# Performance work log

Measured on AMD Instinct MI355X. Metric: run time of the kernel, lower is better.

## Reference

```python
import jax, jax.numpy as jnp
import numpy as np

N_NODES = 200000
N_EDGES = 6400000
IN_DIM = 15      # pfc_input_dim
POS_DIM = 4      # positional_dim
OUT_DIM = 2      # vtx_classes + 1


def setup_inputs() -> dict:
    key = jax.random.key(0)
    k1, k2, k3, k4, k5, k6, k7 = jax.random.split(key, 7)
    x_pfc = jax.random.normal(k1, (N_NODES, IN_DIM), dtype=jnp.float32)
    edge_index = jax.random.randint(k2, (2, N_EDGES), 0, N_NODES, dtype=jnp.int64)
    s_in = 1.0 / np.sqrt(IN_DIM)
    s_pos = 1.0 / np.sqrt(POS_DIM)
    # PointTransformerConv params: lin, lin_src, lin_dst (no bias), pos_nn = Linear(4, 2)
    W_lin = jax.random.uniform(k3, (OUT_DIM, IN_DIM), jnp.float32, -s_in, s_in)
    W_src = jax.random.uniform(k4, (OUT_DIM, IN_DIM), jnp.float32, -s_in, s_in)
    W_dst = jax.random.uniform(k5, (OUT_DIM, IN_DIM), jnp.float32, -s_in, s_in)
    W_pos = jax.random.uniform(k6, (OUT_DIM, POS_DIM), jnp.float32, -s_pos, s_pos)
    b_pos = jax.random.uniform(k7, (OUT_DIM,), jnp.float32, -s_pos, s_pos)
    return {"x_pfc": x_pfc, "edge_index": edge_index, "W_lin": W_lin,
            "W_src": W_src, "W_dst": W_dst, "W_pos": W_pos, "b_pos": b_pos}


def reference(x_pfc, edge_index, W_lin, W_src, W_dst, W_pos, b_pos):
    n = x_pfc.shape[0]
    pos = x_pfc[:, :POS_DIM]
    # original forward calls ptc_only(x, pos, edge_index.flip(0)):
    # source j = edge_index[1], target i = edge_index[0]
    j = edge_index[1]
    i = edge_index[0]
    # node-level linear maps (N x OUT_DIM)
    v = x_pfc @ W_lin.T
    a_src = x_pfc @ W_src.T
    a_dst = x_pfc @ W_dst.T
    # positional MLP on relative positions (E x OUT_DIM)
    delta = (pos[i] - pos[j]) @ W_pos.T + b_pos
    alpha = a_dst[i] - a_src[j] + delta
    # segment softmax over incoming edges of each target node i
    m = jax.ops.segment_max(alpha, i, num_segments=n)  # -inf for empty segments (never indexed)
    e = jnp.exp(alpha - m[i])
    denom = jax.ops.segment_sum(e, i, num_segments=n)
    attn = e / (denom[i] + 1e-16)
    msg = attn * (v[j] + delta)
    return jax.ops.segment_sum(msg, i, num_segments=n)
```

## Files before the change

kernel.cpp:

```cpp
#include <hip/hip_runtime.h>

#define N_NODES 200000
#define N_EDGES 6400000
#define IN_DIM 15
#define POS_DIM 4

#define CSHIFT 9
#define CMASK 511
#define NCOARSE ((N_NODES + 511) >> 9)
#define CHUNK 16384
#define NBLK ((N_EDGES + CHUNK - 1) / CHUNK)
#define CAP 17408

typedef unsigned uv4 __attribute__((ext_vector_type(4)));
typedef int      iv4 __attribute__((ext_vector_type(4)));


__global__ void node_prep(const float* __restrict__ x,
                          const float* __restrict__ Wlin,
                          const float* __restrict__ Wsrc,
                          const float* __restrict__ Wpos,
                          float4* __restrict__ tabJ,
                          unsigned* __restrict__ gcnt)
{
    int n = blockIdx.x * blockDim.x + threadIdx.x;
    if (n < NCOARSE) gcnt[n] = 0u;
    if (n >= N_NODES) return;
    const float* xp = x + (long)n * IN_DIM;
    float xv[IN_DIM];
#pragma unroll
    for (int k = 0; k < IN_DIM; ++k) xv[k] = xp[k];

    float p0 = 0.f, p1 = 0.f;
#pragma unroll
    for (int k = 0; k < POS_DIM; ++k) {
        p0 += Wpos[k] * xv[k];
        p1 += Wpos[POS_DIM + k] * xv[k];
    }
    float v0 = 0.f, v1 = 0.f, as0 = 0.f, as1 = 0.f;
#pragma unroll
    for (int k = 0; k < IN_DIM; ++k) {
        float xk = xv[k];
        v0  += Wlin[k] * xk;  v1  += Wlin[IN_DIM + k] * xk;
        as0 += Wsrc[k] * xk;  as1 += Wsrc[IN_DIM + k] * xk;
    }
    tabJ[n] = make_float4(as0 + p0, as1 + p1, v0 - p0, v1 - p1);
}

__global__ __launch_bounds__(512) void
scatter_kernel(const int* __restrict__ idx,
               unsigned* __restrict__ gcnt,
               unsigned* __restrict__ packed)
{
    __shared__ unsigned stage[CHUNK];
    __shared__ unsigned cnt[512];
    __shared__ unsigned lloc[512];
    __shared__ unsigned gdst[NCOARSE];
    __shared__ unsigned wsum[8];
    int b = blockIdx.x;
    int t = threadIdx.x;
    int lane = t & 63, wid = t >> 6;
    long s0 = (long)b * CHUNK;
    int end = (int)min((long)CHUNK, (long)N_EDGES - s0);
    cnt[t] = 0u;
    __syncthreads();
    iv4 myi[8];
    {
        int rr = 0;
        for (int e = t * 4; e < end; e += 2048, ++rr) {
            iv4 iv = __builtin_nontemporal_load((const iv4*)(idx + s0 + e));
            myi[rr] = iv;
            atomicAdd(&cnt[iv.x >> CSHIFT], 1u);
            atomicAdd(&cnt[iv.y >> CSHIFT], 1u);
            atomicAdd(&cnt[iv.z >> CSHIFT], 1u);
            atomicAdd(&cnt[iv.w >> CSHIFT], 1u);
        }
    }
    __syncthreads();
    unsigned v = cnt[t];
    unsigned s = v;
#pragma unroll
    for (int off = 1; off < 64; off <<= 1) {
        unsigned u = __shfl_up(s, off, 64);
        if (lane >= off) s += u;
    }
    if (lane == 63) wsum[wid] = s;
    __syncthreads();
    unsigned woff = 0;
#pragma unroll
    for (int w = 0; w < 8; ++w) woff += (w < wid) ? wsum[w] : 0u;
    {
        unsigned ex = woff + s - v;
        lloc[t] = ex;
        cnt[t] = ex;
        if (t < NCOARSE) gdst[t] = atomicAdd(&gcnt[t], v);
    }
    __syncthreads();
    {
        int rr = 0;
        for (int e = t * 4; e < end; e += 2048, ++rr) {
            iv4 iv = myi[rr];
            iv4 jv = __builtin_nontemporal_load((const iv4*)(idx + N_EDGES + s0 + e));
            unsigned r0 = atomicAdd(&cnt[iv.x >> CSHIFT], 1u);
            unsigned r1 = atomicAdd(&cnt[iv.y >> CSHIFT], 1u);
            unsigned r2 = atomicAdd(&cnt[iv.z >> CSHIFT], 1u);
            unsigned r3 = atomicAdd(&cnt[iv.w >> CSHIFT], 1u);
            stage[r0] = ((unsigned)jv.x << CSHIFT) | ((unsigned)iv.x & CMASK);
            stage[r1] = ((unsigned)jv.y << CSHIFT) | ((unsigned)iv.y & CMASK);
            stage[r2] = ((unsigned)jv.z << CSHIFT) | ((unsigned)iv.z & CMASK);
            stage[r3] = ((unsigned)jv.w << CSHIFT) | ((unsigned)iv.w & CMASK);
        }
    }
    __syncthreads();
    for (int bk = wid; bk < NCOARSE; bk += 8) {
        unsigned st  = lloc[bk];
        unsigned len = ((bk + 1 < 512) ? lloc[bk + 1] : (unsigned)end) - st;
        unsigned gb  = gdst[bk];
        unsigned rem = (gb < (unsigned)CAP) ? (unsigned)CAP - gb : 0u;
        if (len > rem) len = rem;
        unsigned* dst = packed + (size_t)bk * CAP + gb;
        for (unsigned e = lane; e < len; e += 64u)
            dst[e] = stage[st + e];
    }
}

__global__ __launch_bounds__(1024) void
bucket_agg_kernel(const unsigned* __restrict__ packed,
                  const unsigned* __restrict__ gcnt,
                  const float* __restrict__ x,
                  const float* __restrict__ Wdst,
                  const float* __restrict__ Wpos,
                  const float4* __restrict__ tabJ,
                  const float* __restrict__ bpos,
                  float2* __restrict__ out)
{
    __shared__ unsigned cache[CAP + 512];
    __shared__ unsigned cnt[512], cur[512];
    __shared__ unsigned wsum[8];
    int k = blockIdx.x;
    int t = threadIdx.x;
    int lane = t & 63;
    int r = t >> 1, sub = t & 1;
    float b0 = bpos[0], b1 = bpos[1];
    int gn = (k << CSHIFT) + r;

    float p0 = 0.f, p1 = 0.f, ad0 = 0.f, ad1 = 0.f;
    if (gn < N_NODES) {
        const float* xp = x + (long)gn * IN_DIM;
        float xv[IN_DIM];
#pragma unroll
        for (int q = 0; q < IN_DIM; ++q) xv[q] = xp[q];
#pragma unroll
        for (int q = 0; q < POS_DIM; ++q) {
            p0 += Wpos[q] * xv[q];
            p1 += Wpos[POS_DIM + q] * xv[q];
        }
#pragma unroll
        for (int q = 0; q < IN_DIM; ++q) {
            ad0 += Wdst[q] * xv[q];
            ad1 += Wdst[IN_DIM + q] * xv[q];
        }
    }
    float a0 = ad0 + p0 + b0, a1 = ad1 + p1 + b1;
    float sn0 = 0.f, sn1 = 0.f, sd0 = 0.f, sd1 = 0.f;

    if (t < 512) cnt[t] = 0u;
    __syncthreads();

    unsigned n = min(gcnt[k], (unsigned)CAP);
    const unsigned* pk = packed + (size_t)k * CAP;

    for (unsigned e = 4u * t; e < n; e += 4096u) {
        uv4 p = *(const uv4*)(pk + e);
        atomicAdd(&cnt[p.x & CMASK], 1u);
        if (e + 1 < n) atomicAdd(&cnt[p.y & CMASK], 1u);
        if (e + 2 < n) atomicAdd(&cnt[p.z & CMASK], 1u);
        if (e + 3 < n) atomicAdd(&cnt[p.w & CMASK], 1u);
    }
    __syncthreads();
    unsigned v = 0, s = 0;
    if (t < 512) {
        v = cnt[t];
        s = v;
#pragma unroll
        for (int off = 1; off < 64; off <<= 1) {
            unsigned u = __shfl_up(s, off, 64);
            if (lane >= off) s += u;
        }
        if (lane == 63) wsum[t >> 6] = s;
    }
    __syncthreads();
    if (t < 512) {
        int wid = t >> 6;
        unsigned woff = 0;
#pragma unroll
        for (int w = 0; w < 8; ++w) woff += (w < wid) ? wsum[w] : 0u;
        cur[t] = woff + s - v + (unsigned)t;
    }
    __syncthreads();
    for (unsigned e = 4u * t; e < n; e += 4096u) {
        uv4 p = __builtin_nontemporal_load((const uv4*)(pk + e));
        { unsigned pos = atomicAdd(&cur[p.x & CMASK], 1u); cache[pos] = p.x >> CSHIFT; }
        if (e + 1 < n) { unsigned pos = atomicAdd(&cur[p.y & CMASK], 1u); cache[pos] = p.y >> CSHIFT; }
        if (e + 2 < n) { unsigned pos = atomicAdd(&cur[p.z & CMASK], 1u); cache[pos] = p.z >> CSHIFT; }
        if (e + 3 < n) { unsigned pos = atomicAdd(&cur[p.w & CMASK], 1u); cache[pos] = p.w >> CSHIFT; }
    }
    __syncthreads();
    unsigned deg   = cnt[r];
    unsigned st    = cur[r] - deg;
    unsigned half0 = (deg + 1) >> 1;
    unsigned myst  = st + (sub ? half0 : 0u);
    unsigned mylen = sub ? (deg - half0) : half0;
    unsigned e = 0;
    for (; e + 8u <= mylen; e += 8u) {
        unsigned j0 = cache[myst + e],     j1 = cache[myst + e + 1];
        unsigned j2 = cache[myst + e + 2], j3 = cache[myst + e + 3];
        unsigned j4 = cache[myst + e + 4], j5 = cache[myst + e + 5];
        unsigned j6 = cache[myst + e + 6], j7 = cache[myst + e + 7];
        float4 f0 = tabJ[j0], f1 = tabJ[j1], f2 = tabJ[j2], f3 = tabJ[j3];
        float4 f4 = tabJ[j4], f5 = tabJ[j5], f6 = tabJ[j6], f7 = tabJ[j7];
        float e00 = __expf(a0 - f0.x), e01 = __expf(a1 - f0.y);
        float e10 = __expf(a0 - f1.x), e11 = __expf(a1 - f1.y);
        float e20 = __expf(a0 - f2.x), e21 = __expf(a1 - f2.y);
        float e30 = __expf(a0 - f3.x), e31 = __expf(a1 - f3.y);
        float e40 = __expf(a0 - f4.x), e41 = __expf(a1 - f4.y);
        float e50 = __expf(a0 - f5.x), e51 = __expf(a1 - f5.y);
        float e60 = __expf(a0 - f6.x), e61 = __expf(a1 - f6.y);
        float e70 = __expf(a0 - f7.x), e71 = __expf(a1 - f7.y);
        sn0 += e00 * f0.z + e10 * f1.z + e20 * f2.z + e30 * f3.z
             + e40 * f4.z + e50 * f5.z + e60 * f6.z + e70 * f7.z;
        sn1 += e01 * f0.w + e11 * f1.w + e21 * f2.w + e31 * f3.w
             + e41 * f4.w + e51 * f5.w + e61 * f6.w + e71 * f7.w;
        sd0 += e00 + e10 + e20 + e30 + e40 + e50 + e60 + e70;
        sd1 += e01 + e11 + e21 + e31 + e41 + e51 + e61 + e71;
    }
    for (; e < mylen; ++e) {
        unsigned j = cache[myst + e];
        float4 fj = tabJ[j];
        float e0 = __expf(a0 - fj.x), e1 = __expf(a1 - fj.y);
        sn0 += e0 * fj.z;  sn1 += e1 * fj.w;
        sd0 += e0;         sd1 += e1;
    }
    sn0 += __shfl_xor(sn0, 1);  sn1 += __shfl_xor(sn1, 1);
    sd0 += __shfl_xor(sd0, 1);  sd1 += __shfl_xor(sd1, 1);

    if (sub != 0 || gn >= N_NODES) return;
    float o0 = (sn0 + (p0 + b0) * sd0) / (sd0 + 1e-16f);
    float o1 = (sn1 + (p1 + b1) * sd1) / (sd1 + 1e-16f);
    out[gn] = make_float2(o0, o1);
}

extern "C" void kernel_launch(void* const* d_in, const int* in_sizes, int n_in,
                              void* d_out, int out_size, void* d_ws, size_t ws_size,
                              hipStream_t stream) {
    const float* x    = (const float*)d_in[0];
    const int*   idx  = (const int*)d_in[1];
    const float* Wlin = (const float*)d_in[2];
    const float* Wsrc = (const float*)d_in[3];
    const float* Wdst = (const float*)d_in[4];
    const float* Wpos = (const float*)d_in[5];
    const float* bpos = (const float*)d_in[6];
    float* out = (float*)d_out;

    char* ws = (char*)d_ws;
    size_t off = 0;
    float4* tabJ = (float4*)(ws + off); off += (size_t)N_NODES * 16;
    unsigned* packed = (unsigned*)(ws + off); off += (size_t)NCOARSE * CAP * 4;
    unsigned* gcnt   = (unsigned*)(ws + off); off += (size_t)NCOARSE * 4;

    node_prep<<<(N_NODES + 255) / 256, 256, 0, stream>>>(x, Wlin, Wsrc, Wpos,
                                                         tabJ, gcnt);
    scatter_kernel<<<NBLK, 512, 0, stream>>>(idx, gcnt, packed);
    bucket_agg_kernel<<<NCOARSE, 1024, 0, stream>>>(packed, gcnt,
                                                    x, Wdst, Wpos, tabJ, bpos,
                                                    (float2*)out);
}
```

Measured before the change: 170.0 us.

## Split each aggregation bucket across two blocks and enlarge scatter blocks

Measured after the change: 181.3 us. 1.07x slower.

```diff
diff --git a/kernel.cpp b/kernel.cpp
--- a/kernel.cpp
+++ b/kernel.cpp
@@ -8,9 +8,10 @@
 #define CSHIFT 9
 #define CMASK 511
 #define NCOARSE ((N_NODES + 511) >> 9)
-#define CHUNK 16384
+#define CHUNK 12288
 #define NBLK ((N_EDGES + CHUNK - 1) / CHUNK)
 #define CAP 17408
+#define HCAP 8704
 
 typedef unsigned uv4 __attribute__((ext_vector_type(4)));
 typedef int      iv4 __attribute__((ext_vector_type(4)));
@@ -47,7 +48,7 @@
     tabJ[n] = make_float4(as0 + p0, as1 + p1, v0 - p0, v1 - p1);
 }
 
-__global__ __launch_bounds__(512) void
+__global__ __launch_bounds__(1024) void
 scatter_kernel(const int* __restrict__ idx,
                unsigned* __restrict__ gcnt,
                unsigned* __restrict__ packed)
@@ -62,12 +63,12 @@
     int lane = t & 63, wid = t >> 6;
     long s0 = (long)b * CHUNK;
     int end = (int)min((long)CHUNK, (long)N_EDGES - s0);
-    cnt[t] = 0u;
-    __syncthreads();
-    iv4 myi[8];
+    if (t < 512) cnt[t] = 0u;
+    __syncthreads();
+    iv4 myi[3];
     {
         int rr = 0;
-        for (int e = t * 4; e < end; e += 2048, ++rr) {
+        for (int e = t * 4; e < end; e += 4096, ++rr) {
             iv4 iv = __builtin_nontemporal_load((const iv4*)(idx + s0 + e));
             myi[rr] = iv;
             atomicAdd(&cnt[iv.x >> CSHIFT], 1u);
@@ -77,19 +78,23 @@
         }
     }
     __syncthreads();
-    unsigned v = cnt[t];
-    unsigned s = v;
-#pragma unroll
-    for (int off = 1; off < 64; off <<= 1) {
-        unsigned u = __shfl_up(s, off, 64);
-        if (lane >= off) s += u;
-    }
-    if (lane == 63) wsum[wid] = s;
-    __syncthreads();
-    unsigned woff = 0;
-#pragma unroll
-    for (int w = 0; w < 8; ++w) woff += (w < wid) ? wsum[w] : 0u;
-    {
+    unsigned v = 0, s = 0;
+    if (t < 512) {
+        v = cnt[t];
+        s = v;
+#pragma unroll
+        for (int off = 1; off < 64; off <<= 1) {
+            unsigned u = __shfl_up(s, off, 64);
+            if (lane >= off) s += u;
+        }
+        if (lane == 63) wsum[t >> 6] = s;
+    }
+    __syncthreads();
+    if (t < 512) {
+        int sw = t >> 6;
+        unsigned woff = 0;
+#pragma unroll
+        for (int w = 0; w < 8; ++w) woff += (w < sw) ? wsum[w] : 0u;
         unsigned ex = woff + s - v;
         lloc[t] = ex;
         cnt[t] = ex;
@@ -98,7 +103,7 @@
     __syncthreads();
     {
         int rr = 0;
-        for (int e = t * 4; e < end; e += 2048, ++rr) {
+        for (int e = t * 4; e < end; e += 4096, ++rr) {
             iv4 iv = myi[rr];
             iv4 jv = __builtin_nontemporal_load((const iv4*)(idx + N_EDGES + s0 + e));
             unsigned r0 = atomicAdd(&cnt[iv.x >> CSHIFT], 1u);
@@ -112,9 +117,9 @@
         }
     }
     __syncthreads();
-    for (int bk = wid; bk < NCOARSE; bk += 8) {
+    for (int bk = wid; bk < NCOARSE; bk += 16) {
         unsigned st  = lloc[bk];
-        unsigned len = ((bk + 1 < 512) ? lloc[bk + 1] : (unsigned)end) - st;
+        unsigned len = lloc[bk + 1] - st;
         unsigned gb  = gdst[bk];
         unsigned rem = (gb < (unsigned)CAP) ? (unsigned)CAP - gb : 0u;
         if (len > rem) len = rem;
@@ -124,7 +129,7 @@
     }
 }
 
-__global__ __launch_bounds__(1024) void
+__global__ __launch_bounds__(512) void
 bucket_agg_kernel(const unsigned* __restrict__ packed,
                   const unsigned* __restrict__ gcnt,
                   const float* __restrict__ x,
@@ -134,15 +139,17 @@
                   const float* __restrict__ bpos,
                   float2* __restrict__ out)
 {
-    __shared__ unsigned cache[CAP + 512];
-    __shared__ unsigned cnt[512], cur[512];
-    __shared__ unsigned wsum[8];
-    int k = blockIdx.x;
+    __shared__ unsigned cache[HCAP + 256];
+    __shared__ unsigned cnt[256], cur[256];
+    __shared__ unsigned wsum[4];
+    int blk = blockIdx.x;
+    int k = blk >> 1;
+    unsigned half = (unsigned)(blk & 1);
     int t = threadIdx.x;
     int lane = t & 63;
     int r = t >> 1, sub = t & 1;
     float b0 = bpos[0], b1 = bpos[1];
-    int gn = (k << CSHIFT) + r;
+    int gn = (k << CSHIFT) + ((int)half << 8) + r;
 
     float p0 = 0.f, p1 = 0.f, ad0 = 0.f, ad1 = 0.f;
     if (gn < N_NODES) {
@@ -164,22 +171,23 @@
     float a0 = ad0 + p0 + b0, a1 = ad1 + p1 + b1;
     float sn0 = 0.f, sn1 = 0.f, sd0 = 0.f, sd1 = 0.f;
 
-    if (t < 512) cnt[t] = 0u;
+    if (t < 256) cnt[t] = 0u;
     __syncthreads();
 
     unsigned n = min(gcnt[k], (unsigned)CAP);
     const unsigned* pk = packed + (size_t)k * CAP;
 
-    for (unsigned e = 4u * t; e < n; e += 4096u) {
+#define KEEP(w) ((((w) >> 8) & 1u) == half)
+    for (unsigned e = 4u * t; e < n; e += 2048u) {
         uv4 p = *(const uv4*)(pk + e);
-        atomicAdd(&cnt[p.x & CMASK], 1u);
-        if (e + 1 < n) atomicAdd(&cnt[p.y & CMASK], 1u);
-        if (e + 2 < n) atomicAdd(&cnt[p.z & CMASK], 1u);
-        if (e + 3 < n) atomicAdd(&cnt[p.w & CMASK], 1u);
+        if (KEEP(p.x))               atomicAdd(&cnt[p.x & 255u], 1u);
+        if (e + 1 < n && KEEP(p.y))  atomicAdd(&cnt[p.y & 255u], 1u);
+        if (e + 2 < n && KEEP(p.z))  atomicAdd(&cnt[p.z & 255u], 1u);
+        if (e + 3 < n && KEEP(p.w))  atomicAdd(&cnt[p.w & 255u], 1u);
     }
     __syncthreads();
     unsigned v = 0, s = 0;
-    if (t < 512) {
+    if (t < 256) {
         v = cnt[t];
         s = v;
 #pragma unroll
@@ -190,21 +198,22 @@
         if (lane == 63) wsum[t >> 6] = s;
     }
     __syncthreads();
-    if (t < 512) {
-        int wid = t >> 6;
+    if (t < 256) {
+        int sw = t >> 6;
         unsigned woff = 0;
 #pragma unroll
-        for (int w = 0; w < 8; ++w) woff += (w < wid) ? wsum[w] : 0u;
+        for (int w = 0; w < 4; ++w) woff += (w < sw) ? wsum[w] : 0u;
         cur[t] = woff + s - v + (unsigned)t;
     }
     __syncthreads();
-    for (unsigned e = 4u * t; e < n; e += 4096u) {
-        uv4 p = __builtin_nontemporal_load((const uv4*)(pk + e));
-        { unsigned pos = atomicAdd(&cur[p.x & CMASK], 1u); cache[pos] = p.x >> CSHIFT; }
-        if (e + 1 < n) { unsigned pos = atomicAdd(&cur[p.y & CMASK], 1u); cache[pos] = p.y >> CSHIFT; }
-        if (e + 2 < n) { unsigned pos = atomicAdd(&cur[p.z & CMASK], 1u); cache[pos] = p.z >> CSHIFT; }
-        if (e + 3 < n) { unsigned pos = atomicAdd(&cur[p.w & CMASK], 1u); cache[pos] = p.w >> CSHIFT; }
-    }
+    for (unsigned e = 4u * t; e < n; e += 2048u) {
+        uv4 p = *(const uv4*)(pk + e);
+        if (KEEP(p.x))              { unsigned pos = atomicAdd(&cur[p.x & 255u], 1u); cache[pos] = p.x >> CSHIFT; }
+        if (e + 1 < n && KEEP(p.y)) { unsigned pos = atomicAdd(&cur[p.y & 255u], 1u); cache[pos] = p.y >> CSHIFT; }
+        if (e + 2 < n && KEEP(p.z)) { unsigned pos = atomicAdd(&cur[p.z & 255u], 1u); cache[pos] = p.z >> CSHIFT; }
+        if (e + 3 < n && KEEP(p.w)) { unsigned pos = atomicAdd(&cur[p.w & 255u], 1u); cache[pos] = p.w >> CSHIFT; }
+    }
+#undef KEEP
     __syncthreads();
     unsigned deg   = cnt[r];
     unsigned st    = cur[r] - deg;
@@ -270,8 +279,8 @@
 
     node_prep<<<(N_NODES + 255) / 256, 256, 0, stream>>>(x, Wlin, Wsrc, Wpos,
                                                          tabJ, gcnt);
-    scatter_kernel<<<NBLK, 512, 0, stream>>>(idx, gcnt, packed);
-    bucket_agg_kernel<<<NCOARSE, 1024, 0, stream>>>(packed, gcnt,
-                                                    x, Wdst, Wpos, tabJ, bpos,
-                                                    (float2*)out);
-}
+    scatter_kernel<<<NBLK, 1024, 0, stream>>>(idx, gcnt, packed);
+    bucket_agg_kernel<<<NCOARSE * 2, 512, 0, stream>>>(packed, gcnt,
+                                                       x, Wdst, Wpos, tabJ, bpos,
+                                                       (float2*)out);
+}
```
